# Performance work log

Hardware: AMD Instinct MI355X
Metric: run time of the kernel (lower is better)

Reference implementation:

```python
import jax, jax.numpy as jnp
import numpy as np

NUM_VARS = 256
BATCH = 131072


def setup_inputs() -> dict:
    key = jax.random.key(0)
    k1, k2 = jax.random.split(key)
    z_exogenous = jax.random.normal(k1, (BATCH, NUM_VARS), dtype=jnp.float32)
    # Learnable adjacency parameter; small init like the torch prior (~0.01 scale).
    A_raw = jax.random.normal(k2, (NUM_VARS, NUM_VARS), dtype=jnp.float32) * 0.01
    return {"z_exogenous": z_exogenous, "A_raw": A_raw}


def reference(z_exogenous, A_raw):
    # A = tril(A_raw, -1): strictly lower triangular (no threshold in forward).
    n = A_raw.shape[0]
    A = jnp.tril(A_raw, -1)
    # M = I - A^T is upper triangular with unit diagonal and is shared across
    # the whole batch, so solve the triangular system once for all RHS columns
    # instead of a batched LU (same math as torch.linalg.solve).
    M = jnp.eye(n, dtype=A_raw.dtype) - A.T          # [n, n] upper triangular
    z_causal = jax.scipy.linalg.solve_triangular(M, z_exogenous.T, lower=False).T  # [B, n]
    return z_causal
```

## Files before the change

kernel.cpp:

```cpp
#include <hip/hip_runtime.h>
#include <hip/hip_bf16.h>


typedef __bf16 bf16x8 __attribute__((ext_vector_type(8)));
typedef float f32x4 __attribute__((ext_vector_type(4)));

__device__ __forceinline__ unsigned short f2bf(float f) {
    union { float f; unsigned u; } v; v.f = f;
    unsigned u = v.u;
    u += 0x7FFFu + ((u >> 16) & 1u);
    return (unsigned short)(u >> 16);
}
__device__ __forceinline__ bf16x8 pack8(float4 a, float4 b) {
    union { bf16x8 v; __hip_bfloat162 h[4]; } u;
    u.h[0] = __float22bfloat162_rn(make_float2(a.x, a.y));
    u.h[1] = __float22bfloat162_rn(make_float2(a.z, a.w));
    u.h[2] = __float22bfloat162_rn(make_float2(b.x, b.y));
    u.h[3] = __float22bfloat162_rn(make_float2(b.z, b.w));
    return u.v;
}

#define AST 258
__global__ __launch_bounds__(256) void make_G3(const float* __restrict__ A,
                                               unsigned short* __restrict__ Gt) {
    __shared__ unsigned short As[256 * AST];
    const int tid = threadIdx.x;
    const int l = tid & 63;
    const int wv = tid >> 6;

    for (int it = 0; it < 64; ++it) {
        const int r = it * 4 + wv;
        const int c0 = l * 4;
        float4 v = *(const float4*)(A + r * 256 + c0);
        *(ushort2*)(&As[r * AST + c0])     = make_ushort2(f2bf(v.x), f2bf(v.y));
        *(ushort2*)(&As[r * AST + c0 + 2]) = make_ushort2(f2bf(v.z), f2bf(v.w));
    }
    __syncthreads();
    if (wv != 0) return;

    const int c = blockIdx.x;
    float p[4];
#pragma unroll
    for (int k = 0; k < 4; ++k) p[k] = (64 * k + l == c) ? 1.f : 0.f;

#pragma unroll
    for (int kb = 0; kb < 4; ++kb) {
#pragma unroll 8
        for (int i2 = 0; i2 < 32; ++i2) {
            unsigned u[4];
#pragma unroll
            for (int k = 0; k < 4; ++k)
                if (k >= kb)
                    u[k] = *(const unsigned*)(&As[(64 * k + l) * AST + kb * 64 + 2 * i2]);
            const int t0 = 2 * i2, t1 = t0 + 1;
            float s0 = __int_as_float(__builtin_amdgcn_readlane(__float_as_int(p[kb]), t0));
            p[kb] += (l > t0 ? __int_as_float(u[kb] << 16) : 0.f) * s0;
#pragma unroll
            for (int k = 0; k < 4; ++k)
                if (k > kb) p[k] += __int_as_float(u[k] << 16) * s0;
            float s1 = __int_as_float(__builtin_amdgcn_readlane(__float_as_int(p[kb]), t1));
            p[kb] += (l > t1 ? __int_as_float(u[kb] & 0xffff0000u) : 0.f) * s1;
#pragma unroll
            for (int k = 0; k < 4; ++k)
                if (k > kb) p[k] += __int_as_float(u[k] & 0xffff0000u) * s1;
        }
    }
#pragma unroll
    for (int k = 0; k < 4; ++k)
        Gt[c * 256 + 64 * k + l] = f2bf(p[k]);
}

__global__ __launch_bounds__(512, 4) void scm_gemm4(const float* __restrict__ Z,
                                                    const unsigned short* __restrict__ Gt,
                                                    float* __restrict__ Out) {
    __shared__ __align__(16) unsigned short Gs[128 * 256];
    const int tid = threadIdx.x;
    const int lane = tid & 63;
    const int wave = tid >> 6;
    const int n = lane & 15;
    const int quad = lane >> 4;
    const int bn = (blockIdx.x & 1) * 128;
    const size_t blockRow = (size_t)(blockIdx.x >> 1) * 512;

#pragma unroll
    for (int it = 0; it < 8; ++it) {
        const int chunk = it * 512 + tid;
        const int row = chunk >> 5;
        const int g = chunk & 31;
        const int gs = g ^ (row & 7);
        uint4 v = *(const uint4*)(Gt + (bn + row) * 256 + g * 8);
        *(uint4*)(&Gs[row * 256 + gs * 8]) = v;
    }
    __syncthreads();

    const int swz = n & 7;
    const float* zbase = Z + (blockRow + wave * 16 + n) * 256 + quad * 8;
    float* obase = Out + (blockRow + wave * 16 + quad * 4) * 256 + bn + n;

    f32x4 acc[8];
#pragma unroll
    for (int nt = 0; nt < 8; ++nt) {
        f32x4 zero = {0.f, 0.f, 0.f, 0.f};
        acc[nt] = zero;
    }

    float4 zf[8];
#pragma unroll
    for (int kk = 0; kk < 4; ++kk) {
        zf[2 * kk]     = *(const float4*)(zbase + kk * 32);
        zf[2 * kk + 1] = *(const float4*)(zbase + kk * 32 + 4);
    }

    for (int i = 0; i < 4; ++i) {
        const float* zi = zbase + (size_t)i * 128 * 256;
        bf16x8 af[4];
#pragma unroll
        for (int kk = 0; kk < 4; ++kk) af[kk] = pack8(zf[2 * kk], zf[2 * kk + 1]);
#pragma unroll
        for (int kk = 0; kk < 4; ++kk) {
            zf[2 * kk]     = *(const float4*)(zi + 128 + kk * 32);
            zf[2 * kk + 1] = *(const float4*)(zi + 128 + kk * 32 + 4);
        }
#pragma unroll
        for (int kk = 0; kk < 4; ++kk)
#pragma unroll
            for (int nt = 0; nt < 8; ++nt) {
                const bf16x8 b = *(const bf16x8*)(
                    &Gs[(nt * 16 + n) * 256 + ((kk * 4 + quad) ^ swz) * 8]);
                acc[nt] = __builtin_amdgcn_mfma_f32_16x16x32_bf16(af[kk], b, acc[nt], 0, 0, 0);
            }
#pragma unroll
        for (int kk = 0; kk < 4; ++kk) af[kk] = pack8(zf[2 * kk], zf[2 * kk + 1]);
        if (i < 3) {
            const float* zn = zbase + (size_t)(i + 1) * 128 * 256;
#pragma unroll
            for (int kk = 0; kk < 4; ++kk) {
                zf[2 * kk]     = *(const float4*)(zn + kk * 32);
                zf[2 * kk + 1] = *(const float4*)(zn + kk * 32 + 4);
            }
        }
#pragma unroll
        for (int kk = 0; kk < 4; ++kk)
#pragma unroll
            for (int nt = 0; nt < 8; ++nt) {
                const bf16x8 b = *(const bf16x8*)(
                    &Gs[(nt * 16 + n) * 256 + (((16 + kk * 4 + quad)) ^ swz) * 8]);
                acc[nt] = __builtin_amdgcn_mfma_f32_16x16x32_bf16(af[kk], b, acc[nt], 0, 0, 0);
            }
        float* oi = obase + (size_t)i * 128 * 256;
#pragma unroll
        for (int nt = 0; nt < 8; ++nt)
#pragma unroll
            for (int r = 0; r < 4; ++r) {
                oi[(size_t)r * 256 + nt * 16] = acc[nt][r];
                acc[nt][r] = 0.f;
            }
    }
}

extern "C" void kernel_launch(void* const* d_in, const int* in_sizes, int n_in,
                              void* d_out, int out_size, void* d_ws, size_t ws_size,
                              hipStream_t stream) {
    const float* Z = (const float*)d_in[0];
    const float* A = (const float*)d_in[1];
    float* Out = (float*)d_out;
    unsigned short* Gt = (unsigned short*)d_ws;

    hipLaunchKernelGGL(make_G3, dim3(256), dim3(256), 0, stream, A, Gt);
    hipLaunchKernelGGL(scm_gemm4, dim3(512), dim3(512), 0, stream, Z, Gt, Out);
}
```

Before: 265.8 us.

## Software-pipeline Z loads per k-step with inline asm and explicit vmcnt waits

```diff
diff --git a/kernel.cpp b/kernel.cpp
--- a/kernel.cpp
+++ b/kernel.cpp
@@ -70,7 +70,37 @@
         Gt[c * 256 + 64 * k + l] = f2bf(p[k]);
 }
 
-__global__ __launch_bounds__(512, 4) void scm_gemm4(const float* __restrict__ Z,
+template<int T>
+__device__ __forceinline__ void phaseT(float4& a0, float4& a1,
+                                       const float* zbase, f32x4 acc[8],
+                                       const unsigned short* Gsp,
+                                       int n, int quad, int swz) {
+    constexpr int q = T & 7;
+    constexpr int CNT = (T < 8)   ? 6
+                      : (T == 29) ? 4
+                      : (T == 30) ? 2
+                      : (T == 31) ? 0
+                      : (q < 4 ? 38 : 6);
+    asm volatile("s_waitcnt vmcnt(%0)" :: "n"(CNT) : "memory");
+    __builtin_amdgcn_sched_barrier(0);
+    bf16x8 af = pack8(a0, a1);
+    if constexpr (T + 4 < 32) {
+        constexpr int TT = T + 4;
+        const float* pz = zbase + (size_t)(TT >> 3) * 32768;
+        asm volatile("global_load_dwordx4 %0, %1, off offset:%2"
+                     : "=v"(a0) : "v"(pz), "n"((TT & 7) * 128));
+        asm volatile("global_load_dwordx4 %0, %1, off offset:%2"
+                     : "=v"(a1) : "v"(pz), "n"((TT & 7) * 128 + 16));
+    }
+#pragma unroll
+    for (int nt = 0; nt < 8; ++nt) {
+        const bf16x8 b = *(const bf16x8*)(
+            &Gsp[(nt * 16 + n) * 256 + ((q * 4 + quad) ^ swz) * 8]);
+        acc[nt] = __builtin_amdgcn_mfma_f32_16x16x32_bf16(af, b, acc[nt], 0, 0, 0);
+    }
+}
+
+__global__ __launch_bounds__(512, 4) void scm_gemm8(const float* __restrict__ Z,
                                                     const unsigned short* __restrict__ Gt,
                                                     float* __restrict__ Out) {
     __shared__ __align__(16) unsigned short Gs[128 * 256];
@@ -105,57 +135,41 @@
     }
 
     float4 zf[8];
-#pragma unroll
-    for (int kk = 0; kk < 4; ++kk) {
-        zf[2 * kk]     = *(const float4*)(zbase + kk * 32);
-        zf[2 * kk + 1] = *(const float4*)(zbase + kk * 32 + 4);
+    asm volatile("global_load_dwordx4 %0, %1, off offset:0"   : "=v"(zf[0]) : "v"(zbase));
+    asm volatile("global_load_dwordx4 %0, %1, off offset:16"  : "=v"(zf[1]) : "v"(zbase));
+    asm volatile("global_load_dwordx4 %0, %1, off offset:128" : "=v"(zf[2]) : "v"(zbase));
+    asm volatile("global_load_dwordx4 %0, %1, off offset:144" : "=v"(zf[3]) : "v"(zbase));
+    asm volatile("global_load_dwordx4 %0, %1, off offset:256" : "=v"(zf[4]) : "v"(zbase));
+    asm volatile("global_load_dwordx4 %0, %1, off offset:272" : "=v"(zf[5]) : "v"(zbase));
+    asm volatile("global_load_dwordx4 %0, %1, off offset:384" : "=v"(zf[6]) : "v"(zbase));
+    asm volatile("global_load_dwordx4 %0, %1, off offset:400" : "=v"(zf[7]) : "v"(zbase));
+
+#define PH(T) phaseT<T>(zf[2 * ((T) & 3)], zf[2 * ((T) & 3) + 1], zbase, acc, Gs, n, quad, swz)
+#define STORE_ITER(i, REZERO)                                              \
+    {                                                                      \
+        asm volatile("" ::: "memory");                                     \
+        float* oi = obase + (size_t)(i) * 32768;                           \
+        _Pragma("unroll")                                                  \
+        for (int nt = 0; nt < 8; ++nt)                                     \
+            _Pragma("unroll")                                              \
+            for (int r = 0; r < 4; ++r) {                                  \
+                oi[(size_t)r * 256 + nt * 16] = acc[nt][r];                \
+                if (REZERO) acc[nt][r] = 0.f;                              \
+            }                                                              \
+        asm volatile("" ::: "memory");                                     \
     }
 
-    for (int i = 0; i < 4; ++i) {
-        const float* zi = zbase + (size_t)i * 128 * 256;
-        bf16x8 af[4];
-#pragma unroll
-        for (int kk = 0; kk < 4; ++kk) af[kk] = pack8(zf[2 * kk], zf[2 * kk + 1]);
-#pragma unroll
-        for (int kk = 0; kk < 4; ++kk) {
-            zf[2 * kk]     = *(const float4*)(zi + 128 + kk * 32);
-            zf[2 * kk + 1] = *(const float4*)(zi + 128 + kk * 32 + 4);
-        }
-#pragma unroll
-        for (int kk = 0; kk < 4; ++kk)
-#pragma unroll
-            for (int nt = 0; nt < 8; ++nt) {
-                const bf16x8 b = *(const bf16x8*)(
-                    &Gs[(nt * 16 + n) * 256 + ((kk * 4 + quad) ^ swz) * 8]);
-                acc[nt] = __builtin_amdgcn_mfma_f32_16x16x32_bf16(af[kk], b, acc[nt], 0, 0, 0);
-            }
-#pragma unroll
-        for (int kk = 0; kk < 4; ++kk) af[kk] = pack8(zf[2 * kk], zf[2 * kk + 1]);
-        if (i < 3) {
-            const float* zn = zbase + (size_t)(i + 1) * 128 * 256;
-#pragma unroll
-            for (int kk = 0; kk < 4; ++kk) {
-                zf[2 * kk]     = *(const float4*)(zn + kk * 32);
-                zf[2 * kk + 1] = *(const float4*)(zn + kk * 32 + 4);
-            }
-        }
-#pragma unroll
-        for (int kk = 0; kk < 4; ++kk)
-#pragma unroll
-            for (int nt = 0; nt < 8; ++nt) {
-                const bf16x8 b = *(const bf16x8*)(
-                    &Gs[(nt * 16 + n) * 256 + (((16 + kk * 4 + quad)) ^ swz) * 8]);
-                acc[nt] = __builtin_amdgcn_mfma_f32_16x16x32_bf16(af[kk], b, acc[nt], 0, 0, 0);
-            }
-        float* oi = obase + (size_t)i * 128 * 256;
-#pragma unroll
-        for (int nt = 0; nt < 8; ++nt)
-#pragma unroll
-            for (int r = 0; r < 4; ++r) {
-                oi[(size_t)r * 256 + nt * 16] = acc[nt][r];
-                acc[nt][r] = 0.f;
-            }
-    }
+    PH(0);  PH(1);  PH(2);  PH(3);  PH(4);  PH(5);  PH(6);  PH(7);
+    STORE_ITER(0, true);
+    PH(8);  PH(9);  PH(10); PH(11); PH(12); PH(13); PH(14); PH(15);
+    STORE_ITER(1, true);
+    PH(16); PH(17); PH(18); PH(19); PH(20); PH(21); PH(22); PH(23);
+    STORE_ITER(2, true);
+    PH(24); PH(25); PH(26); PH(27); PH(28); PH(29); PH(30); PH(31);
+    STORE_ITER(3, false);
+
+#undef PH
+#undef STORE_ITER
 }
 
 extern "C" void kernel_launch(void* const* d_in, const int* in_sizes, int n_in,
@@ -167,5 +181,5 @@
     unsigned short* Gt = (unsigned short*)d_ws;
 
     hipLaunchKernelGGL(make_G3, dim3(256), dim3(256), 0, stream, A, Gt);
-    hipLaunchKernelGGL(scm_gemm4, dim3(512), dim3(512), 0, stream, Z, Gt, Out);
+    hipLaunchKernelGGL(scm_gemm8, dim3(512), dim3(512), 0, stream, Z, Gt, Out);
 }
```

Result: no change. 266.7 us (+0.4%).
